# Kernel optimization log

Hardware: AMD Instinct MI355X
Metric: run time of the kernel (lower is better)

Reference implementation:

```python
import jax, jax.numpy as jnp
import numpy as np

BATCH, INPUT_SIZE, ALPHA_DIM = 512, 64, 64


def fast_logexpmv(A, B):
    """Log-semiring matmul: C[b,i,j] = logsumexp_k A[b,i,k] + B[b,k,j], numerically stable."""
    a_max = jnp.max(A, axis=-1, keepdims=True)   # (B, i, 1)
    b_max = jnp.max(B, axis=-2, keepdims=True)   # (B, 1, j)
    C = jnp.log(jnp.matmul(jnp.exp(A - a_max), jnp.exp(B - b_max)))
    return C + a_max + b_max


def setup_inputs() -> dict:
    key = jax.random.key(0)
    k1, k2, k3 = jax.random.split(key, 3)
    x = jax.random.bernoulli(k1, 0.5, (BATCH, INPUT_SIZE)).astype(jnp.float32)
    theta = jax.random.uniform(k2, (1, INPUT_SIZE, ALPHA_DIM, ALPHA_DIM), dtype=jnp.float32)
    u_log_p_alpha = jax.random.normal(k3, (1, INPUT_SIZE - 1, 1, ALPHA_DIM), dtype=jnp.float32)
    return {"x": x, "theta": theta, "u_log_p_alpha": u_log_p_alpha}


def reference(x, theta, u_log_p_alpha):
    # normalized log p(alpha) over last dim (matches _log_p_alpha's manual logsumexp)
    log_p_alpha = jax.nn.log_softmax(u_log_p_alpha, axis=-1)          # (1, T-1, 1, a)
    # per-position Bernoulli log-likelihood matrices:
    # -clamp(theta,0) + theta*x - log(1 + exp(-|theta|))  -> (B, T, a, a)
    log_px_mats = (-jnp.clip(theta, 0.0)
                   + theta * x[:, :, None, None]
                   - jnp.log1p(jnp.exp(-jnp.abs(theta))))
    joint = log_px_mats[:, :-1] + log_p_alpha                          # (B, T-1, a, a)
    mats = jnp.transpose(joint, (1, 0, 2, 3))                          # (T-1, B, a, a)

    def step(carry, m):
        return fast_logexpmv(carry, m), None

    left, _ = jax.lax.scan(step, mats[0], mats[1:])                    # (B, a, a)
    p_xn_g_alpha_n1 = log_px_mats[:, -1, :, 0:1]                       # (B, a, 1)
    log_px = fast_logexpmv(left, p_xn_g_alpha_n1)                      # (B, a, 1)
    return log_px
```

## Files before the change

kernel.cpp:

```cpp
#include <hip/hip_runtime.h>
#include <hip/hip_bf16.h>


#define NSTEP 63

typedef __attribute__((ext_vector_type(8)))  short short8;
typedef __attribute__((ext_vector_type(16))) float f32x16;

union U8 { short8 v; unsigned u[4]; unsigned short s[8]; };

static __device__ __forceinline__ unsigned short bf16b(float f) {
  union { __hip_bfloat16 h; unsigned short u; } cv;
  cv.h = __float2bfloat16(f);
  return cv.u;
}
static __device__ __forceinline__ unsigned pack2(float a, float b) {
  return (unsigned)bf16b(a) | ((unsigned)bf16b(b) << 16);
}

__global__ __launch_bounds__(256) void e_kernel(
    const float* __restrict__ theta, const float* __restrict__ ulpa,
    unsigned short* __restrict__ EA, unsigned short* __restrict__ EB) {
  int t = blockIdx.x;
  int tid = threadIdx.x;
  __shared__ float sig[64][65];
  __shared__ float pa[64];

  if (tid < 64) {
    float u = ulpa[t * 64 + tid];
    float m = u;
    #pragma unroll
    for (int o = 32; o >= 1; o >>= 1) m = fmaxf(m, __shfl_xor(m, o));
    float e = __expf(u - m);
    float s = e;
    #pragma unroll
    for (int o = 32; o >= 1; o >>= 1) s += __shfl_xor(s, o);
    pa[tid] = e / s;
  }

  const float4* th4 = (const float4*)(theta + t * 4096);
  #pragma unroll
  for (int k = 0; k < 4; ++k) {
    int i = tid + k * 256;
    float4 v = th4[i];
    int m = i >> 4, n0 = (i & 15) * 4;
    sig[m][n0 + 0] = 1.0f / (1.0f + __expf(-v.x));
    sig[m][n0 + 1] = 1.0f / (1.0f + __expf(-v.y));
    sig[m][n0 + 2] = 1.0f / (1.0f + __expf(-v.z));
    sig[m][n0 + 3] = 1.0f / (1.0f + __expf(-v.w));
  }
  __syncthreads();

  unsigned short* EA0 = EA + (size_t)(t * 2 + 0) * 4096;
  unsigned short* EA1 = EA + (size_t)(t * 2 + 1) * 4096;
  unsigned short* EB0 = EB + (size_t)(t * 2 + 0) * 4096;
  unsigned short* EB1 = EB + (size_t)(t * 2 + 1) * 4096;

  #pragma unroll
  for (int k = 0; k < 4; ++k) {
    int i = tid + k * 256;
    int m = i >> 4, n0 = (i & 15) * 4;
    float p0 = pa[n0], p1 = pa[n0 + 1], p2 = pa[n0 + 2], p3 = pa[n0 + 3];
    float s0 = sig[m][n0], s1 = sig[m][n0 + 1];
    float s2 = sig[m][n0 + 2], s3 = sig[m][n0 + 3];
    *reinterpret_cast<uint2*>(&EA1[m * 64 + n0]) =
        make_uint2(pack2(s0 * p0, s1 * p1), pack2(s2 * p2, s3 * p3));
    *reinterpret_cast<uint2*>(&EA0[m * 64 + n0]) =
        make_uint2(pack2((1.0f - s0) * p0, (1.0f - s1) * p1),
                   pack2((1.0f - s2) * p2, (1.0f - s3) * p3));
  }
  #pragma unroll
  for (int k = 0; k < 4; ++k) {
    int i = tid + k * 256;
    int n = i >> 4, m0 = (i & 15) * 4;
    float pn = pa[n];
    float s0 = sig[m0][n], s1 = sig[m0 + 1][n];
    float s2 = sig[m0 + 2][n], s3 = sig[m0 + 3][n];
    *reinterpret_cast<uint2*>(&EB1[n * 64 + m0]) =
        make_uint2(pack2(s0 * pn, s1 * pn), pack2(s2 * pn, s3 * pn));
    *reinterpret_cast<uint2*>(&EB0[n * 64 + m0]) =
        make_uint2(pack2((1.0f - s0) * pn, (1.0f - s1) * pn),
                   pack2((1.0f - s2) * pn, (1.0f - s3) * pn));
  }
}

static __device__ __forceinline__ void mm64(const short8 A[4][2],
                                            const short8 B[4][2],
                                            f32x16 C[2][2]) {
  #pragma unroll
  for (int ti = 0; ti < 2; ++ti)
    #pragma unroll
    for (int j = 0; j < 2; ++j)
      #pragma unroll
      for (int r = 0; r < 16; ++r) C[ti][j][r] = 0.0f;
  #pragma unroll
  for (int kc = 0; kc < 4; ++kc)
    #pragma unroll
    for (int j = 0; j < 2; ++j)
      #pragma unroll
      for (int ti = 0; ti < 2; ++ti)
        C[ti][j] = __builtin_amdgcn_mfma_f32_32x32x16_bf16(
            A[kc][ti], B[kc][j], C[ti][j], 0, 0, 0);
}

static __device__ __forceinline__ void loadA_g(short8 A[4][2],
                                               const unsigned short* M,
                                               int lo, int hi) {
  #pragma unroll
  for (int kc = 0; kc < 4; ++kc)
    #pragma unroll
    for (int ti = 0; ti < 2; ++ti)
      A[kc][ti] = *reinterpret_cast<const short8*>(
          &M[(32 * ti + lo) * 64 + 16 * kc + 8 * hi]);
}
static __device__ __forceinline__ void loadB_g(short8 B[4][2],
                                               const unsigned short* M,
                                               int lo, int hi) {
  #pragma unroll
  for (int kc = 0; kc < 4; ++kc)
    #pragma unroll
    for (int j = 0; j < 2; ++j)
      B[kc][j] = *reinterpret_cast<const short8*>(
          &M[(32 * j + lo) * 64 + 16 * kc + 8 * hi]);
}

static __device__ __forceinline__ void store_role(const f32x16 C[2][2],
                                                  char* base, int role,
                                                  int lo, int hi) {
  if (role == 0) {
    #pragma unroll
    for (int ti = 0; ti < 2; ++ti)
      #pragma unroll
      for (int j = 0; j < 2; ++j)
        #pragma unroll
        for (int r = 0; r < 16; ++r) {
          int m = 32 * ti + (r & 3) + 8 * (r >> 2) + 4 * hi;
          int n = 32 * j + lo;
          unsigned byteoff =
              ((unsigned)(m * 128 + n * 2)) ^ ((unsigned)(m & 7) << 4);
          *reinterpret_cast<unsigned short*>(base + byteoff) =
              bf16b(C[ti][j][r]);
        }
  } else {
    #pragma unroll
    for (int ti = 0; ti < 2; ++ti)
      #pragma unroll
      for (int j = 0; j < 2; ++j)
        #pragma unroll
        for (int rq = 0; rq < 4; ++rq) {
          int n = 32 * j + lo;
          int mb = 32 * ti + 8 * rq + 4 * hi;
          unsigned byteoff =
              ((unsigned)(n * 128 + mb * 2)) ^ ((unsigned)(n & 7) << 4);
          uint2 wv = make_uint2(
              pack2(C[ti][j][4 * rq + 0], C[ti][j][4 * rq + 1]),
              pack2(C[ti][j][4 * rq + 2], C[ti][j][4 * rq + 3]));
          *reinterpret_cast<uint2*>(base + byteoff) = wv;
        }
  }
}

static __device__ __forceinline__ void loadA_lds(short8 A[4][2],
                                                 const char* base,
                                                 int lo, int hi) {
  #pragma unroll
  for (int kc = 0; kc < 4; ++kc)
    #pragma unroll
    for (int ti = 0; ti < 2; ++ti) {
      int m = 32 * ti + lo;
      unsigned byteoff = ((unsigned)(m * 128 + (16 * kc + 8 * hi) * 2)) ^
                         ((unsigned)(m & 7) << 4);
      A[kc][ti] = *reinterpret_cast<const short8*>(base + byteoff);
    }
}
static __device__ __forceinline__ void loadB_lds(short8 B[4][2],
                                                 const char* base,
                                                 int lo, int hi) {
  #pragma unroll
  for (int kc = 0; kc < 4; ++kc)
    #pragma unroll
    for (int j = 0; j < 2; ++j) {
      int n = 32 * j + lo;
      unsigned byteoff = ((unsigned)(n * 128 + (16 * kc + 8 * hi) * 2)) ^
                         ((unsigned)(n & 7) << 4);
      B[kc][j] = *reinterpret_cast<const short8*>(base + byteoff);
    }
}

static __device__ __forceinline__ void rebuildB(const f32x16 C[2][2],
                                                short8 B[4][2], int hi) {
  #pragma unroll
  for (int kc = 0; kc < 4; ++kc) {
    int Me = 2 * kc, Mo = 2 * kc + 1;
    int tie = Me >> 2, me = Me & 3;
    int tio = Mo >> 2, mo = Mo & 3;
    #pragma unroll
    for (int j = 0; j < 2; ++j) {
      unsigned pe0 = pack2(C[tie][j][4 * me + 0], C[tie][j][4 * me + 1]);
      unsigned pe1 = pack2(C[tie][j][4 * me + 2], C[tie][j][4 * me + 3]);
      unsigned po0 = pack2(C[tio][j][4 * mo + 0], C[tio][j][4 * mo + 1]);
      unsigned po1 = pack2(C[tio][j][4 * mo + 2], C[tio][j][4 * mo + 3]);
      unsigned s0 = hi ? pe0 : po0;
      unsigned s1 = hi ? pe1 : po1;
      unsigned r0 = (unsigned)__shfl_xor((int)s0, 32);
      unsigned r1 = (unsigned)__shfl_xor((int)s1, 32);
      U8 f;
      f.u[0] = hi ? r0 : pe0;
      f.u[1] = hi ? r1 : pe1;
      f.u[2] = hi ? po0 : r0;
      f.u[3] = hi ? po1 : r1;
      B[kc][j] = f.v;
    }
  }
}

__global__ __launch_bounds__(64) void quad_kernel(
    const unsigned short* __restrict__ EA, const unsigned short* __restrict__ EB,
    unsigned short* __restrict__ MqB) {
  __shared__ __align__(16) char Lsh[8192];

  int bid = blockIdx.x;
  int lane = threadIdx.x, lo = lane & 31, hi = lane >> 5;
  int v, nt, t0, g;
  if (bid < 240) { v = bid & 15; nt = 4; g = bid >> 4; t0 = 4 * g; }
  else           { v = bid - 240; nt = 3; g = 15; t0 = 60; }

  short8 A[4][2], B[4][2];
  f32x16 C1[2][2], C2[2][2], C3[2][2];

  if (nt == 4) {
    int b0 = v & 1, b1 = (v >> 1) & 1, b2 = (v >> 2) & 1, b3 = (v >> 3) & 1;
    loadA_g(A, EB + (size_t)((t0 + 3) * 2 + b3) * 4096, lo, hi);
    loadB_g(B, EA + (size_t)((t0 + 2) * 2 + b2) * 4096, lo, hi);
    mm64(A, B, C1);
    loadA_g(A, EB + (size_t)((t0 + 1) * 2 + b1) * 4096, lo, hi);
    loadB_g(B, EA + (size_t)((t0 + 0) * 2 + b0) * 4096, lo, hi);
    mm64(A, B, C2);
    store_role(C1, Lsh, 0, lo, hi);
    loadA_lds(A, Lsh, lo, hi);
    rebuildB(C2, B, hi);
    mm64(A, B, C3);
  } else {
    int b0 = v & 1, b1 = (v >> 1) & 1, b2 = (v >> 2) & 1;
    loadA_g(A, EB + (size_t)((t0 + 2) * 2 + b2) * 4096, lo, hi);
    loadB_g(B, EA + (size_t)((t0 + 1) * 2 + b1) * 4096, lo, hi);
    mm64(A, B, C1);
    store_role(C1, Lsh, 0, lo, hi);
    loadA_lds(A, Lsh, lo, hi);
    loadB_g(B, EA + (size_t)((t0 + 0) * 2 + b0) * 4096, lo, hi);
    mm64(A, B, C3);
  }

  unsigned short* outp = MqB + (size_t)bid * 4096;
  if ((g & 1) == 0) {
    #pragma unroll
    for (int ti = 0; ti < 2; ++ti)
      #pragma unroll
      for (int j = 0; j < 2; ++j)
        #pragma unroll
        for (int rq = 0; rq < 4; ++rq) {
          int n = 32 * j + lo;
          int mb = 32 * ti + 8 * rq + 4 * hi;
          uint2 wv = make_uint2(
              pack2(C3[ti][j][4 * rq + 0], C3[ti][j][4 * rq + 1]),
              pack2(C3[ti][j][4 * rq + 2], C3[ti][j][4 * rq + 3]));
          *reinterpret_cast<uint2*>(&outp[n * 64 + mb]) = wv;
        }
  } else {
    #pragma unroll
    for (int ti = 0; ti < 2; ++ti)
      #pragma unroll
      for (int j = 0; j < 2; ++j)
        #pragma unroll
        for (int r = 0; r < 16; ++r) {
          int m = 32 * ti + (r & 3) + 8 * (r >> 2) + 4 * hi;
          int n = 32 * j + lo;
          outp[m * 64 + n] = bf16b(C3[ti][j][r]);
        }
  }
}

__global__ __launch_bounds__(512, 2) void tree_kernel(
    const float* __restrict__ x, const float* __restrict__ theta,
    const unsigned short* __restrict__ MqB, float* __restrict__ out) {
  __shared__ __align__(16) char Lsh[8 * 8192];

  int b = blockIdx.x, tid = threadIdx.x;
  int w = tid >> 6, lane = tid & 63, lo = lane & 31, hi = lane >> 5;

  unsigned long long mask = __ballot(x[b * 64 + lane] != 0.0f);

#define GIDX(g) ((g) < 15 ? (g) * 16 + (int)((mask >> (4 * (g))) & 15ull) \
                          : 240 + (int)((mask >> 60) & 7ull))

  short8 A[4][2], B[4][2];
  f32x16 C[2][2];

  {
    const unsigned short* GA = MqB + (size_t)GIDX(2 * w) * 4096;
    const unsigned short* GB = MqB + (size_t)GIDX(2 * w + 1) * 4096;
    loadA_g(A, GA, lo, hi);
    loadB_g(B, GB, lo, hi);
    mm64(A, B, C);
    store_role(C, Lsh + w * 8192, w & 1, lo, hi);
  }
  __syncthreads();

  if (w < 4)
    { loadA_lds(A, Lsh + (2 * w) * 8192, lo, hi);
      loadB_lds(B, Lsh + (2 * w + 1) * 8192, lo, hi); }
  __syncthreads();
  if (w < 4) {
    mm64(A, B, C);
    store_role(C, Lsh + w * 8192, w & 1, lo, hi);
  }
  __syncthreads();

  if (w < 2)
    { loadA_lds(A, Lsh + (2 * w) * 8192, lo, hi);
      loadB_lds(B, Lsh + (2 * w + 1) * 8192, lo, hi); }
  __syncthreads();
  if (w < 2) {
    mm64(A, B, C);
    store_role(C, Lsh + w * 8192, w & 1, lo, hi);
  }
  __syncthreads();

  if (w == 0) {
    loadA_lds(A, Lsh + 0, lo, hi);
    loadB_lds(B, Lsh + 8192, lo, hi);
    mm64(A, B, C);

    float* lf = reinterpret_cast<float*>(Lsh);
    #pragma unroll
    for (int ti = 0; ti < 2; ++ti)
      #pragma unroll
      for (int j = 0; j < 2; ++j)
        #pragma unroll
        for (int r = 0; r < 16; ++r) {
          int m = 32 * ti + (r & 3) + 8 * (r >> 2) + 4 * hi;
          int n = 32 * j + lo;
          lf[(n >> 2) * 256 + m * 4 + (n & 3)] = C[ti][j][r];
        }

    float th = theta[63 * 4096 + lane * 64];
    float sg = 1.0f / (1.0f + __expf(-th));
    float* u = lf + 4096;
    u[lane] = ((mask >> 63) & 1ull) ? sg : (1.0f - sg);

    const float4* Qm4 = reinterpret_cast<const float4*>(lf);
    float s0 = 0.f, s1 = 0.f, s2 = 0.f, s3 = 0.f;
    #pragma unroll
    for (int gq = 0; gq < 16; gq += 4) {
      float4 q0 = Qm4[(gq + 0) * 64 + lane];
      float4 q1 = Qm4[(gq + 1) * 64 + lane];
      float4 q2 = Qm4[(gq + 2) * 64 + lane];
      float4 q3 = Qm4[(gq + 3) * 64 + lane];
      float4 u0 = *(const float4*)&u[(gq + 0) * 4];
      float4 u1 = *(const float4*)&u[(gq + 1) * 4];
      float4 u2 = *(const float4*)&u[(gq + 2) * 4];
      float4 u3 = *(const float4*)&u[(gq + 3) * 4];
      s0 = fmaf(q0.x, u0.x, s0); s0 = fmaf(q0.y, u0.y, s0);
      s0 = fmaf(q0.z, u0.z, s0); s0 = fmaf(q0.w, u0.w, s0);
      s1 = fmaf(q1.x, u1.x, s1); s1 = fmaf(q1.y, u1.y, s1);
      s1 = fmaf(q1.z, u1.z, s1); s1 = fmaf(q1.w, u1.w, s1);
      s2 = fmaf(q2.x, u2.x, s2); s2 = fmaf(q2.y, u2.y, s2);
      s2 = fmaf(q2.z, u2.z, s2); s2 = fmaf(q2.w, u2.w, s2);
      s3 = fmaf(q3.x, u3.x, s3); s3 = fmaf(q3.y, u3.y, s3);
      s3 = fmaf(q3.z, u3.z, s3); s3 = fmaf(q3.w, u3.w, s3);
    }
    float s = (s0 + s1) + (s2 + s3);
    out[b * 64 + lane] = logf(s);
  }
#undef GIDX
}

extern "C" void kernel_launch(void* const* d_in, const int* in_sizes, int n_in,
                              void* d_out, int out_size, void* d_ws, size_t ws_size,
                              hipStream_t stream) {
  const float* x     = (const float*)d_in[0];
  const float* theta = (const float*)d_in[1];
  const float* ulpa  = (const float*)d_in[2];
  float* out = (float*)d_out;

  unsigned short* MqB = (unsigned short*)d_ws;
  unsigned short* EA  = MqB + (size_t)248 * 4096;
  unsigned short* EB  = EA + (size_t)NSTEP * 2 * 4096;

  hipLaunchKernelGGL(e_kernel, dim3(NSTEP), dim3(256), 0, stream,
                     theta, ulpa, EA, EB);
  hipLaunchKernelGGL(quad_kernel, dim3(248), dim3(64), 0, stream,
                     EA, EB, MqB);
  hipLaunchKernelGGL(tree_kernel, dim3(512), dim3(512), 0, stream,
                     x, theta, MqB, out);
}
```

Measured before the change: 85.87 us.

## Replace per-batch matrix tree reduction with right-to-left matrix-vector chain

The final per-batch stage used to multiply 16 precomputed 64x64 quad matrices pairwise in a tree of MFMA matmuls across 8 waves. It now keeps a vector and applies the 16 matrices one at a time as matrix-vector products in a single wave, prefetching the next matrix into registers. The quad outputs are stored in a column-blocked bf16 layout so each lane can load its row with vector loads. This removes most of the matmul FLOPs, the LDS traffic and the block-wide barriers. In exchange the chain is fully serial, and one midway max-rescale is added to limit overflow.

```diff
diff --git a/kernel.cpp b/kernel.cpp
--- a/kernel.cpp
+++ b/kernel.cpp
@@ -16,6 +16,9 @@
 }
 static __device__ __forceinline__ unsigned pack2(float a, float b) {
   return (unsigned)bf16b(a) | ((unsigned)bf16b(b) << 16);
+}
+static __device__ __forceinline__ float bfcvt(unsigned short s) {
+  return __uint_as_float((unsigned)s << 16);
 }
 
 __global__ __launch_bounds__(256) void e_kernel(
@@ -124,40 +127,20 @@
           &M[(32 * j + lo) * 64 + 16 * kc + 8 * hi]);
 }
 
-static __device__ __forceinline__ void store_role(const f32x16 C[2][2],
-                                                  char* base, int role,
-                                                  int lo, int hi) {
-  if (role == 0) {
-    #pragma unroll
-    for (int ti = 0; ti < 2; ++ti)
+static __device__ __forceinline__ void store_role0(const f32x16 C[2][2],
+                                                   char* base, int lo, int hi) {
+  #pragma unroll
+  for (int ti = 0; ti < 2; ++ti)
+    #pragma unroll
+    for (int j = 0; j < 2; ++j)
       #pragma unroll
-      for (int j = 0; j < 2; ++j)
-        #pragma unroll
-        for (int r = 0; r < 16; ++r) {
-          int m = 32 * ti + (r & 3) + 8 * (r >> 2) + 4 * hi;
-          int n = 32 * j + lo;
-          unsigned byteoff =
-              ((unsigned)(m * 128 + n * 2)) ^ ((unsigned)(m & 7) << 4);
-          *reinterpret_cast<unsigned short*>(base + byteoff) =
-              bf16b(C[ti][j][r]);
-        }
-  } else {
-    #pragma unroll
-    for (int ti = 0; ti < 2; ++ti)
-      #pragma unroll
-      for (int j = 0; j < 2; ++j)
-        #pragma unroll
-        for (int rq = 0; rq < 4; ++rq) {
-          int n = 32 * j + lo;
-          int mb = 32 * ti + 8 * rq + 4 * hi;
-          unsigned byteoff =
-              ((unsigned)(n * 128 + mb * 2)) ^ ((unsigned)(n & 7) << 4);
-          uint2 wv = make_uint2(
-              pack2(C[ti][j][4 * rq + 0], C[ti][j][4 * rq + 1]),
-              pack2(C[ti][j][4 * rq + 2], C[ti][j][4 * rq + 3]));
-          *reinterpret_cast<uint2*>(base + byteoff) = wv;
-        }
-  }
+      for (int r = 0; r < 16; ++r) {
+        int m = 32 * ti + (r & 3) + 8 * (r >> 2) + 4 * hi;
+        int n = 32 * j + lo;
+        unsigned byteoff =
+            ((unsigned)(m * 128 + n * 2)) ^ ((unsigned)(m & 7) << 4);
+        *reinterpret_cast<unsigned short*>(base + byteoff) = bf16b(C[ti][j][r]);
+      }
 }
 
 static __device__ __forceinline__ void loadA_lds(short8 A[4][2],
@@ -171,19 +154,6 @@
       unsigned byteoff = ((unsigned)(m * 128 + (16 * kc + 8 * hi) * 2)) ^
                          ((unsigned)(m & 7) << 4);
       A[kc][ti] = *reinterpret_cast<const short8*>(base + byteoff);
-    }
-}
-static __device__ __forceinline__ void loadB_lds(short8 B[4][2],
-                                                 const char* base,
-                                                 int lo, int hi) {
-  #pragma unroll
-  for (int kc = 0; kc < 4; ++kc)
-    #pragma unroll
-    for (int j = 0; j < 2; ++j) {
-      int n = 32 * j + lo;
-      unsigned byteoff = ((unsigned)(n * 128 + (16 * kc + 8 * hi) * 2)) ^
-                         ((unsigned)(n & 7) << 4);
-      B[kc][j] = *reinterpret_cast<const short8*>(base + byteoff);
     }
 }
 
@@ -216,14 +186,14 @@
 
 __global__ __launch_bounds__(64) void quad_kernel(
     const unsigned short* __restrict__ EA, const unsigned short* __restrict__ EB,
-    unsigned short* __restrict__ MqB) {
+    unsigned short* __restrict__ MqC) {
   __shared__ __align__(16) char Lsh[8192];
 
   int bid = blockIdx.x;
   int lane = threadIdx.x, lo = lane & 31, hi = lane >> 5;
-  int v, nt, t0, g;
-  if (bid < 240) { v = bid & 15; nt = 4; g = bid >> 4; t0 = 4 * g; }
-  else           { v = bid - 240; nt = 3; g = 15; t0 = 60; }
+  int v, nt, t0;
+  if (bid < 240) { v = bid & 15; nt = 4; t0 = 4 * (bid >> 4); }
+  else           { v = bid - 240; nt = 3; t0 = 60; }
 
   short8 A[4][2], B[4][2];
   f32x16 C1[2][2], C2[2][2], C3[2][2];
@@ -236,7 +206,7 @@
     loadA_g(A, EB + (size_t)((t0 + 1) * 2 + b1) * 4096, lo, hi);
     loadB_g(B, EA + (size_t)((t0 + 0) * 2 + b0) * 4096, lo, hi);
     mm64(A, B, C2);
-    store_role(C1, Lsh, 0, lo, hi);
+    store_role0(C1, Lsh, lo, hi);
     loadA_lds(A, Lsh, lo, hi);
     rebuildB(C2, B, hi);
     mm64(A, B, C3);
@@ -245,134 +215,109 @@
     loadA_g(A, EB + (size_t)((t0 + 2) * 2 + b2) * 4096, lo, hi);
     loadB_g(B, EA + (size_t)((t0 + 1) * 2 + b1) * 4096, lo, hi);
     mm64(A, B, C1);
-    store_role(C1, Lsh, 0, lo, hi);
+    store_role0(C1, Lsh, lo, hi);
     loadA_lds(A, Lsh, lo, hi);
     loadB_g(B, EA + (size_t)((t0 + 0) * 2 + b0) * 4096, lo, hi);
     mm64(A, B, C3);
   }
 
-  unsigned short* outp = MqB + (size_t)bid * 4096;
-  if ((g & 1) == 0) {
-    #pragma unroll
-    for (int ti = 0; ti < 2; ++ti)
+  unsigned short* outp = MqC + (size_t)bid * 4096;
+  #pragma unroll
+  for (int ti = 0; ti < 2; ++ti)
+    #pragma unroll
+    for (int j = 0; j < 2; ++j)
       #pragma unroll
-      for (int j = 0; j < 2; ++j)
-        #pragma unroll
-        for (int rq = 0; rq < 4; ++rq) {
-          int n = 32 * j + lo;
-          int mb = 32 * ti + 8 * rq + 4 * hi;
-          uint2 wv = make_uint2(
-              pack2(C3[ti][j][4 * rq + 0], C3[ti][j][4 * rq + 1]),
-              pack2(C3[ti][j][4 * rq + 2], C3[ti][j][4 * rq + 3]));
-          *reinterpret_cast<uint2*>(&outp[n * 64 + mb]) = wv;
-        }
-  } else {
-    #pragma unroll
-    for (int ti = 0; ti < 2; ++ti)
-      #pragma unroll
-      for (int j = 0; j < 2; ++j)
-        #pragma unroll
-        for (int r = 0; r < 16; ++r) {
-          int m = 32 * ti + (r & 3) + 8 * (r >> 2) + 4 * hi;
-          int n = 32 * j + lo;
-          outp[m * 64 + n] = bf16b(C3[ti][j][r]);
-        }
-  }
-}
-
-__global__ __launch_bounds__(512, 2) void tree_kernel(
+      for (int r = 0; r < 16; ++r) {
+        int m = 32 * ti + (r & 3) + 8 * (r >> 2) + 4 * hi;
+        int n = 32 * j + lo;
+        outp[(m >> 3) * 512 + n * 8 + (m & 7)] = bf16b(C3[ti][j][r]);
+      }
+}
+
+__global__ __launch_bounds__(64) void chain_kernel(
     const float* __restrict__ x, const float* __restrict__ theta,
-    const unsigned short* __restrict__ MqB, float* __restrict__ out) {
-  __shared__ __align__(16) char Lsh[8 * 8192];
-
-  int b = blockIdx.x, tid = threadIdx.x;
-  int w = tid >> 6, lane = tid & 63, lo = lane & 31, hi = lane >> 5;
+    const unsigned short* __restrict__ MqC, float* __restrict__ out) {
+  int b = blockIdx.x;
+  int lane = threadIdx.x;
 
   unsigned long long mask = __ballot(x[b * 64 + lane] != 0.0f);
+
+  __shared__ __align__(16) float u_lds[64];
+
+  float th = theta[63 * 4096 + lane * 64];
+  float sg = 1.0f / (1.0f + __expf(-th));
+  float u = ((mask >> 63) & 1ull) ? sg : (1.0f - sg);
+  float acc = 0.0f;
 
 #define GIDX(g) ((g) < 15 ? (g) * 16 + (int)((mask >> (4 * (g))) & 15ull) \
                           : 240 + (int)((mask >> 60) & 7ull))
 
-  short8 A[4][2], B[4][2];
-  f32x16 C[2][2];
+  short8 qa[8], qb[8], qc[8];
+
+#define PRE(REG, PG)                                                      \
+  {                                                                       \
+    const unsigned short* Pb = MqC + (size_t)GIDX(PG) * 4096 + lane * 8;  \
+    _Pragma("unroll")                                                     \
+    for (int gi = 0; gi < 8; ++gi)                                        \
+      REG[gi] = *reinterpret_cast<const short8*>(Pb + gi * 512);          \
+  }
+
+#define STEP(QREG, PG, PREG)                                              \
+  {                                                                       \
+    u_lds[lane] = u;                                                      \
+    if ((PG) >= 0) PRE(PREG, PG);                                         \
+    float s0 = 0.f, s1 = 0.f, s2 = 0.f, s3 = 0.f;                         \
+    _Pragma("unroll")                                                     \
+    for (int gi = 0; gi < 8; ++gi) {                                      \
+      U8 f; f.v = QREG[gi];                                               \
+      float4 uu0 = *(const float4*)&u_lds[gi * 8];                        \
+      float4 uu1 = *(const float4*)&u_lds[gi * 8 + 4];                    \
+      s0 = fmaf(bfcvt(f.s[0]), uu0.x, s0);                                \
+      s1 = fmaf(bfcvt(f.s[1]), uu0.y, s1);                                \
+      s2 = fmaf(bfcvt(f.s[2]), uu0.z, s2);                                \
+      s3 = fmaf(bfcvt(f.s[3]), uu0.w, s3);                                \
+      s0 = fmaf(bfcvt(f.s[4]), uu1.x, s0);                                \
+      s1 = fmaf(bfcvt(f.s[5]), uu1.y, s1);                                \
+      s2 = fmaf(bfcvt(f.s[6]), uu1.z, s2);                                \
+      s3 = fmaf(bfcvt(f.s[7]), uu1.w, s3);                                \
+    }                                                                     \
+    u = (s0 + s1) + (s2 + s3);                                            \
+  }
+
+  PRE(qa, 15);
+  PRE(qb, 14);
+
+  STEP(qa, 13, qc);
+  STEP(qb, 12, qa);
+  STEP(qc, 11, qb);
+  STEP(qa, 10, qc);
+  STEP(qb,  9, qa);
+  STEP(qc,  8, qb);
+  STEP(qa,  7, qc);
+  STEP(qb,  6, qa);
 
   {
-    const unsigned short* GA = MqB + (size_t)GIDX(2 * w) * 4096;
-    const unsigned short* GB = MqB + (size_t)GIDX(2 * w + 1) * 4096;
-    loadA_g(A, GA, lo, hi);
-    loadB_g(B, GB, lo, hi);
-    mm64(A, B, C);
-    store_role(C, Lsh + w * 8192, w & 1, lo, hi);
-  }
-  __syncthreads();
-
-  if (w < 4)
-    { loadA_lds(A, Lsh + (2 * w) * 8192, lo, hi);
-      loadB_lds(B, Lsh + (2 * w + 1) * 8192, lo, hi); }
-  __syncthreads();
-  if (w < 4) {
-    mm64(A, B, C);
-    store_role(C, Lsh + w * 8192, w & 1, lo, hi);
-  }
-  __syncthreads();
-
-  if (w < 2)
-    { loadA_lds(A, Lsh + (2 * w) * 8192, lo, hi);
-      loadB_lds(B, Lsh + (2 * w + 1) * 8192, lo, hi); }
-  __syncthreads();
-  if (w < 2) {
-    mm64(A, B, C);
-    store_role(C, Lsh + w * 8192, w & 1, lo, hi);
-  }
-  __syncthreads();
-
-  if (w == 0) {
-    loadA_lds(A, Lsh + 0, lo, hi);
-    loadB_lds(B, Lsh + 8192, lo, hi);
-    mm64(A, B, C);
-
-    float* lf = reinterpret_cast<float*>(Lsh);
-    #pragma unroll
-    for (int ti = 0; ti < 2; ++ti)
-      #pragma unroll
-      for (int j = 0; j < 2; ++j)
-        #pragma unroll
-        for (int r = 0; r < 16; ++r) {
-          int m = 32 * ti + (r & 3) + 8 * (r >> 2) + 4 * hi;
-          int n = 32 * j + lo;
-          lf[(n >> 2) * 256 + m * 4 + (n & 3)] = C[ti][j][r];
-        }
-
-    float th = theta[63 * 4096 + lane * 64];
-    float sg = 1.0f / (1.0f + __expf(-th));
-    float* u = lf + 4096;
-    u[lane] = ((mask >> 63) & 1ull) ? sg : (1.0f - sg);
-
-    const float4* Qm4 = reinterpret_cast<const float4*>(lf);
-    float s0 = 0.f, s1 = 0.f, s2 = 0.f, s3 = 0.f;
-    #pragma unroll
-    for (int gq = 0; gq < 16; gq += 4) {
-      float4 q0 = Qm4[(gq + 0) * 64 + lane];
-      float4 q1 = Qm4[(gq + 1) * 64 + lane];
-      float4 q2 = Qm4[(gq + 2) * 64 + lane];
-      float4 q3 = Qm4[(gq + 3) * 64 + lane];
-      float4 u0 = *(const float4*)&u[(gq + 0) * 4];
-      float4 u1 = *(const float4*)&u[(gq + 1) * 4];
-      float4 u2 = *(const float4*)&u[(gq + 2) * 4];
-      float4 u3 = *(const float4*)&u[(gq + 3) * 4];
-      s0 = fmaf(q0.x, u0.x, s0); s0 = fmaf(q0.y, u0.y, s0);
-      s0 = fmaf(q0.z, u0.z, s0); s0 = fmaf(q0.w, u0.w, s0);
-      s1 = fmaf(q1.x, u1.x, s1); s1 = fmaf(q1.y, u1.y, s1);
-      s1 = fmaf(q1.z, u1.z, s1); s1 = fmaf(q1.w, u1.w, s1);
-      s2 = fmaf(q2.x, u2.x, s2); s2 = fmaf(q2.y, u2.y, s2);
-      s2 = fmaf(q2.z, u2.z, s2); s2 = fmaf(q2.w, u2.w, s2);
-      s3 = fmaf(q3.x, u3.x, s3); s3 = fmaf(q3.y, u3.y, s3);
-      s3 = fmaf(q3.z, u3.z, s3); s3 = fmaf(q3.w, u3.w, s3);
-    }
-    float s = (s0 + s1) + (s2 + s3);
-    out[b * 64 + lane] = logf(s);
-  }
+    float m = u;
+    #pragma unroll
+    for (int o = 32; o >= 1; o >>= 1) m = fmaxf(m, __shfl_xor(m, o));
+    acc += __logf(m);
+    u *= (1.0f / m);
+  }
+
+  STEP(qc,  5, qb);
+  STEP(qa,  4, qc);
+  STEP(qb,  3, qa);
+  STEP(qc,  2, qb);
+  STEP(qa,  1, qc);
+  STEP(qb,  0, qa);
+  STEP(qc, -1, qb);
+  STEP(qa, -1, qb);
+
+#undef STEP
+#undef PRE
 #undef GIDX
+
+  out[b * 64 + lane] = logf(u) + acc;
 }
 
 extern "C" void kernel_launch(void* const* d_in, const int* in_sizes, int n_in,
@@ -383,14 +328,14 @@
   const float* ulpa  = (const float*)d_in[2];
   float* out = (float*)d_out;
 
-  unsigned short* MqB = (unsigned short*)d_ws;
-  unsigned short* EA  = MqB + (size_t)248 * 4096;
+  unsigned short* MqC = (unsigned short*)d_ws;
+  unsigned short* EA  = MqC + (size_t)248 * 4096;
   unsigned short* EB  = EA + (size_t)NSTEP * 2 * 4096;
 
   hipLaunchKernelGGL(e_kernel, dim3(NSTEP), dim3(256), 0, stream,
                      theta, ulpa, EA, EB);
   hipLaunchKernelGGL(quad_kernel, dim3(248), dim3(64), 0, stream,
-                     EA, EB, MqB);
-  hipLaunchKernelGGL(tree_kernel, dim3(512), dim3(512), 0, stream,
-                     x, theta, MqB, out);
-}
+                     EA, EB, MqC);
+  hipLaunchKernelGGL(chain_kernel, dim3(512), dim3(64), 0, stream,
+                     x, theta, MqC, out);
+}
```

New measurement: 76.12 us. 1.13x faster.
